# Kernel optimization log

Measured on AMD Instinct MI355X. Metric: run time of the kernel, lower is better.

The kernel has to match this reference:

```python
import jax, jax.numpy as jnp
import numpy as np

D_MODEL = 768
D_STATE = 16
D_CONV = 4
EXPAND = 2
D_INNER = EXPAND * D_MODEL  # 1536
BATCH = 2
SEQLEN = 4096


def setup_inputs() -> dict:
    key = jax.random.key(0)
    ks = jax.random.split(key, 8)
    s = 0.02
    return {
        "hidden_states": jax.random.normal(ks[0], (BATCH, SEQLEN, D_MODEL), jnp.float32),
        "W_in": jax.random.normal(ks[1], (D_MODEL, 2 * D_INNER), jnp.float32) * s,
        "conv_w": jax.random.normal(ks[2], (D_INNER, 1, D_CONV), jnp.float32) * s,
        "conv_b": jnp.zeros((D_INNER,), jnp.float32),
        "W_x": jax.random.normal(ks[3], (D_INNER, 2 * D_STATE + D_INNER), jnp.float32) * s,
        "W_dt": jax.random.normal(ks[4], (D_INNER, D_INNER), jnp.float32) * s,
        "b_dt": jnp.zeros((D_INNER,), jnp.float32),
        "A_log": jax.random.uniform(ks[5], (D_INNER, D_STATE), jnp.float32, minval=-1.0, maxval=0.0),
        "D": jnp.ones((D_INNER,), jnp.float32),
        "W_out": jax.random.normal(ks[6], (D_INNER, D_MODEL), jnp.float32) * s,
    }


def _silu(x):
    return x * jax.nn.sigmoid(x)


def reference(hidden_states, W_in, conv_w, conv_b, W_x, W_dt, b_dt, A_log, D, W_out):
    B, L, _ = hidden_states.shape
    # in_proj and split into x / gate z  (torch splits first half -> x, second -> z)
    xz = hidden_states @ W_in                      # (B, L, 2*ed)
    x, z = xz[..., :D_INNER], xz[..., D_INNER:]
    # causal depthwise conv1d (torch pads d_conv-1 both sides then truncates to L == left pad)
    xc = jnp.swapaxes(x, 1, 2)                     # (B, ed, L)
    xc = jax.lax.conv_general_dilated(
        xc, conv_w, window_strides=(1,), padding=[(D_CONV - 1, 0)],
        dimension_numbers=("NCH", "OIH", "NCH"), feature_group_count=D_INNER)
    x = jnp.swapaxes(xc, 1, 2) + conv_b            # (B, L, ed)
    x = _silu(x)
    # input-dependent SSM params
    xp = x @ W_x                                   # (B, L, 2*ds + ed)
    Bm = jax.nn.softmax(xp[..., :D_STATE], axis=-1)          # (B, L, ds)
    Cm = xp[..., D_STATE:2 * D_STATE]                          # (B, L, ds)
    delta = jax.nn.softplus(xp[..., 2 * D_STATE:] @ W_dt + b_dt)  # (B, L, ed)
    A = -jnp.exp(A_log.astype(jnp.float32))        # (ed, ds)

    def step(h, t):
        dt, Bt, Ct, ut = t                         # (B,ed),(B,ds),(B,ds),(B,ed)
        dA = jnp.exp(dt[:, :, None] * A)           # (B, ed, ds)
        h = dA * h + (dt[:, :, None] * Bt[:, None, :]) * ut[:, :, None]
        y = jnp.einsum('bs,bds->bd', Ct, h)        # (B, ed)
        return h, y

    h0 = jnp.zeros((B, D_INNER, D_STATE), x.dtype)
    ts = (jnp.swapaxes(delta, 0, 1), jnp.swapaxes(Bm, 0, 1),
          jnp.swapaxes(Cm, 0, 1), jnp.swapaxes(x, 0, 1))
    _, ys = jax.lax.scan(step, h0, ts)             # ys: (L, B, ed)
    y = jnp.swapaxes(ys, 0, 1)                     # (B, L, ed)
    # gating + out projection (torch fallback path does NOT add D * u)
    y = y * _silu(z)
    return y @ W_out
```

## Files before the change

### kernel.cpp

```cpp
#include <hip/hip_runtime.h>
#include <hip/hip_bf16.h>
#include <math.h>

#define D_MODEL 768
#define D_STATE 16
#define D_CONVW 4
#define D_INNER 1536
#define BATCH   2
#define SEQLEN  4096
#define NROWS   (BATCH*SEQLEN)
#define NCHUNK  128
#define LCHUNK  (SEQLEN/NCHUNK)

typedef __attribute__((ext_vector_type(8))) short short8;
typedef __attribute__((ext_vector_type(4))) float floatx4;

__device__ inline unsigned short f2b(float x) {
    unsigned u = __float_as_uint(x);
    return (unsigned short)((u + 0x7fffu + ((u >> 16) & 1u)) >> 16);
}
__device__ inline float b2f(unsigned short b) {
    return __uint_as_float(((unsigned)b) << 16);
}

#define GLDS(gp, lp) __builtin_amdgcn_global_load_lds( \
    (const __attribute__((address_space(1))) void*)(gp), \
    (__attribute__((address_space(3))) void*)(lp), 16, 0, 0)

template<int EPI, int OUTBF16>
__global__ __launch_bounds__(256, 4) void gemm_p2(
    const unsigned short* __restrict__ A, int lda,
    const unsigned short* __restrict__ Bt, int ldb,
    void* __restrict__ Cv, int ldc, float* __restrict__ C2,
    int N, int K, const float* __restrict__ bias, int nbx)
{
    __shared__ unsigned short As0[128*32], As1[128*32];
    __shared__ unsigned short Bs0[128*32], Bs1[128*32];

    const int nwg = gridDim.x;
    const int cpx = nwg >> 3;
    const int wg  = blockIdx.x;
    const int xcd = wg & 7, local = wg >> 3;
    int bmi, bni;
    if ((cpx % nbx == 0) && ((nbx & 1) == 0)) {
        const int R   = cpx / nbx;
        const int p   = local / (2 * R);
        const int idx = local % (2 * R);
        bmi = xcd * R + (idx >> 1);
        bni = p * 2 + (idx & 1);
    } else {
        const int swz = xcd * cpx + local;
        bmi = swz / nbx;
        bni = swz % nbx;
    }
    const int bm = bmi * 128;
    const int bn = bni * 128;

    const int tid  = threadIdx.x;
    const int lane = tid & 63;
    const int wave = tid >> 6;
    const int wm   = (wave >> 1) * 64;
    const int wn   = (wave & 1) * 64;
    const int l15  = lane & 15;
    const int lg   = lane >> 4;

    const int sr    = tid >> 2;
    const int sg    = ((tid & 3) ^ ((tid >> 3) & 3)) * 8;
    const int lbase = (tid & ~63) * 16;

    floatx4 acc[4][4] = {};

    auto stagePair = [&](unsigned short (&SA)[128*32],
                         unsigned short (&SB)[128*32], int kt) {
        #pragma unroll
        for (int p = 0; p < 2; ++p) {
            const unsigned short* ga = A + (size_t)(bm + p * 64 + sr) * lda + kt + sg;
            GLDS(ga, (char*)SA + p * 4096 + lbase);
        }
        #pragma unroll
        for (int p = 0; p < 2; ++p) {
            const unsigned short* gb = Bt + (size_t)(bn + p * 64 + sr) * ldb + kt + sg;
            GLDS(gb, (char*)SB + p * 4096 + lbase);
        }
    };

    auto compute = [&](const unsigned short (&CA)[128*32],
                       const unsigned short (&CB)[128*32]) {
        short8 af[4], bfv[4];
        #pragma unroll
        for (int i = 0; i < 4; ++i) {
            const int tr = wm + i * 16 + l15;
            const int ge = lg ^ ((tr >> 1) & 3);
            af[i] = *(const short8*)((const char*)CA + tr * 64 + ge * 16);
        }
        #pragma unroll
        for (int j = 0; j < 4; ++j) {
            const int tr = wn + j * 16 + l15;
            const int ge = lg ^ ((tr >> 1) & 3);
            bfv[j] = *(const short8*)((const char*)CB + tr * 64 + ge * 16);
        }
        #pragma unroll
        for (int i = 0; i < 4; ++i)
            #pragma unroll
            for (int j = 0; j < 4; ++j)
                acc[i][j] = __builtin_amdgcn_mfma_f32_16x16x32_bf16(
                    af[i], bfv[j], acc[i][j], 0, 0, 0);
    };

    const int NT = K >> 5;

    stagePair(As0, Bs0, 0);

    #define STEP(SA, SB, CA, CB, T)                                          \
    {                                                                        \
        const int t_ = (T);                                                  \
        if (t_ + 1 < NT) {                                                   \
            stagePair(SA, SB, (t_ + 1) * 32);                                \
            asm volatile("s_waitcnt vmcnt(4)" ::: "memory");                 \
        } else {                                                             \
            asm volatile("s_waitcnt vmcnt(0)" ::: "memory");                 \
        }                                                                    \
        __builtin_amdgcn_sched_barrier(0);                                   \
        __builtin_amdgcn_s_barrier();                                        \
        __builtin_amdgcn_sched_barrier(0);                                   \
        compute(CA, CB);                                                     \
        __builtin_amdgcn_sched_barrier(0);                                   \
        __builtin_amdgcn_s_barrier();                                        \
        __builtin_amdgcn_sched_barrier(0);                                   \
    }

    for (int t = 0; t < NT; t += 2) {
        STEP(As1, Bs1, As0, Bs0, t);
        STEP(As0, Bs0, As1, Bs1, t + 1);
    }
    #undef STEP

    #pragma unroll
    for (int i = 0; i < 4; ++i) {
        #pragma unroll
        for (int r = 0; r < 4; ++r) {
            const int gm = bm + wm + i * 16 + lg * 4 + r;
            #pragma unroll
            for (int j = 0; j < 4; ++j) {
                const int gn = bn + wn + j * 16 + l15;
                float v = acc[i][j][r];
                if (EPI == 3) {
                    if (gn < 32) {
                        C2[(size_t)gm * 32 + gn] = v;
                    } else if (gn < N) {
                        v += bias[gn - 32];
                        v = (v > 20.f) ? v : log1pf(__expf(v));
                        ((unsigned short*)Cv)[(size_t)gm * 1536 + gn - 32] = f2b(v);
                    }
                } else {
                    if (gn < N) {
                        if (OUTBF16)
                            ((unsigned short*)Cv)[(size_t)gm * ldc + gn] = f2b(v);
                        else
                            ((float*)Cv)[(size_t)gm * ldc + gn] = v;
                    }
                }
            }
        }
    }
}

__global__ __launch_bounds__(256) void transpose_bf16(
    const float* __restrict__ W, unsigned short* __restrict__ Wt, int K, int N)
{
    __shared__ float t[32][33];
    const int nt = blockIdx.x * 32, kt = blockIdx.y * 32;
    const int tx = threadIdx.x & 31, ty = threadIdx.x >> 5;
    #pragma unroll
    for (int r = 0; r < 4; ++r) {
        const int k = ty + r * 8;
        const int n = nt + tx;
        float v = 0.f;
        if (n < N) v = W[(size_t)(kt + k) * N + n];
        t[k][tx] = v;
    }
    __syncthreads();
    #pragma unroll
    for (int r = 0; r < 4; ++r) {
        const int nl = ty + r * 8;
        Wt[(size_t)(nt + nl) * K + kt + tx] = f2b(t[tx][nl]);
    }
}

__global__ __launch_bounds__(256) void f32_to_bf16(
    const float* __restrict__ in, unsigned short* __restrict__ o, int n4)
{
    const int i = blockIdx.x * 256 + threadIdx.x;
    if (i >= n4) return;
    float4 v = ((const float4*)in)[i];
    ushort4 r;
    r.x = f2b(v.x); r.y = f2b(v.y); r.z = f2b(v.z); r.w = f2b(v.w);
    ((ushort4*)o)[i] = r;
}

__global__ __launch_bounds__(256) void wx32_to_bf16(
    const float* __restrict__ Wx, unsigned short* __restrict__ o)
{
    const int i = blockIdx.x * 256 + threadIdx.x;
    if (i >= 1536 * 384) return;
    const int row = i / 384, q = i % 384;
    float4 v = *(const float4*)(Wx + (size_t)row * 1568 + 32 + q * 4);
    ushort4 r;
    r.x = f2b(v.x); r.y = f2b(v.y); r.z = f2b(v.z); r.w = f2b(v.w);
    *(ushort4*)(o + (size_t)row * 1536 + q * 4) = r;
}

__global__ __launch_bounds__(256) void conv_silu8(
    const unsigned short* __restrict__ xzb, const float* __restrict__ w,
    const float* __restrict__ cb, unsigned short* __restrict__ ub)
{
    const int i = blockIdx.x * 256 + threadIdx.x;
    if (i >= NROWS * 192) return;
    const int g   = i % 192;
    const int row = i / 192;
    const int l   = row % SEQLEN;
    const int d0  = g * 8;

    short8 xr[4];
    #pragma unroll
    for (int k = 0; k < 4; ++k) {
        const int ll = l - 3 + k;
        if (ll >= 0)
            xr[k] = *(const short8*)&xzb[(size_t)(row - 3 + k) * 3072 + d0];
        else
            xr[k] = short8{0,0,0,0,0,0,0,0};
    }
    unsigned short o[8];
    #pragma unroll
    for (int e = 0; e < 8; ++e) {
        float4 we = *(const float4*)&w[(d0 + e) * 4];
        float a = cb[d0 + e];
        a = fmaf(b2f((unsigned short)xr[0][e]), we.x, a);
        a = fmaf(b2f((unsigned short)xr[1][e]), we.y, a);
        a = fmaf(b2f((unsigned short)xr[2][e]), we.z, a);
        a = fmaf(b2f((unsigned short)xr[3][e]), we.w, a);
        o[e] = f2b(a / (1.f + __expf(-a)));
    }
    *(short8*)&ub[(size_t)row * 1536 + d0] = *(short8*)o;
}

__global__ __launch_bounds__(256) void softmax_bc_kernel(
    const float* __restrict__ xp32, float* __restrict__ Bsm, float* __restrict__ Csm)
{
    const int row = blockIdx.x * 256 + threadIdx.x;
    if (row >= NROWS) return;
    const float* p = xp32 + (size_t)row * 32;
    float v[16];
    #pragma unroll
    for (int q = 0; q < 4; ++q) {
        float4 t = *(const float4*)(p + q * 4);
        v[q*4+0]=t.x; v[q*4+1]=t.y; v[q*4+2]=t.z; v[q*4+3]=t.w;
    }
    float mx = v[0];
    #pragma unroll
    for (int s = 1; s < 16; ++s) mx = fmaxf(mx, v[s]);
    float sum = 0.f;
    #pragma unroll
    for (int s = 0; s < 16; ++s) { v[s] = __expf(v[s] - mx); sum += v[s]; }
    const float inv = 1.f / sum;
    float* bo = Bsm + (size_t)row * 16;
    float* co = Csm + (size_t)row * 16;
    #pragma unroll
    for (int s = 0; s < 16; ++s) bo[s] = v[s] * inv;
    #pragma unroll
    for (int q = 0; q < 4; ++q)
        *(float4*)(co + q * 4) = *(const float4*)(p + 16 + q * 4);
}

__global__ __launch_bounds__(256) void scan_chunk_state(
    const unsigned short* __restrict__ deltab, const unsigned short* __restrict__ ub,
    const float* __restrict__ Bsm, const float* __restrict__ A_log,
    float* __restrict__ chunkS, float* __restrict__ dtsum)
{
    const int gid = blockIdx.x * 256 + threadIdx.x;
    const int d = gid % D_INNER;
    const int c = (gid / D_INNER) % NCHUNK;
    const int b = gid / (D_INNER * NCHUNK);

    float A2[16];
    #pragma unroll
    for (int q = 0; q < 4; ++q) {
        float4 t = *(const float4*)(A_log + d * 16 + q * 4);
        A2[q*4+0] = -__expf(t.x) * 1.44269504089f;
        A2[q*4+1] = -__expf(t.y) * 1.44269504089f;
        A2[q*4+2] = -__expf(t.z) * 1.44269504089f;
        A2[q*4+3] = -__expf(t.w) * 1.44269504089f;
    }
    float h[16];
    #pragma unroll
    for (int s = 0; s < 16; ++s) h[s] = 0.f;
    float dts = 0.f;

    const int t0 = c * LCHUNK;
    for (int t = t0; t < t0 + LCHUNK; ++t) {
        const size_t rowoff = (size_t)b * SEQLEN + t;
        const float dt = b2f(deltab[rowoff * D_INNER + d]);
        const float uu = b2f(ub[rowoff * D_INNER + d]);
        const float du = dt * uu;
        dts += dt;
        const float4* Bp = (const float4*)(Bsm + rowoff * 16);
        float Bv[16];
        #pragma unroll
        for (int q = 0; q < 4; ++q) {
            float4 tb = Bp[q];
            Bv[q*4+0]=tb.x; Bv[q*4+1]=tb.y; Bv[q*4+2]=tb.z; Bv[q*4+3]=tb.w;
        }
        #pragma unroll
        for (int s = 0; s < 16; ++s) {
            const float dA = exp2f(dt * A2[s]);
            h[s] = fmaf(dA, h[s], du * Bv[s]);
        }
    }
    float* S = chunkS + (size_t)gid * 16;
    #pragma unroll
    for (int q = 0; q < 4; ++q)
        *(float4*)(S + q * 4) = make_float4(h[q*4+0], h[q*4+1], h[q*4+2], h[q*4+3]);
    dtsum[gid] = dts;
}

__global__ __launch_bounds__(256) void scan_chunk_scan(
    const float* __restrict__ A_log, const float* __restrict__ dtsum,
    float* __restrict__ chunkS)
{
    const int gid = blockIdx.x * 256 + threadIdx.x;
    if (gid >= BATCH * D_INNER * 16) return;
    const int s = gid % 16;
    const int d = (gid / 16) % D_INNER;
    const int b = gid / (16 * D_INNER);
    const float A2 = -__expf(A_log[d * 16 + s]) * 1.44269504089f;
    float hprev = 0.f;
    for (int c = 0; c < NCHUNK; ++c) {
        const size_t cidx = ((size_t)(b * NCHUNK + c) * D_INNER + d);
        const float P  = exp2f(A2 * dtsum[cidx]);
        const size_t idx = cidx * 16 + s;
        const float Sc = chunkS[idx];
        chunkS[idx] = hprev;
        hprev = fmaf(P, hprev, Sc);
    }
}

__global__ __launch_bounds__(256) void scan_output(
    const unsigned short* __restrict__ deltab, const unsigned short* __restrict__ ub,
    const float* __restrict__ Bsm, const float* __restrict__ Csm,
    const float* __restrict__ A_log, const float* __restrict__ chunkS,
    const unsigned short* __restrict__ xzb, unsigned short* __restrict__ yb)
{
    const int gid = blockIdx.x * 256 + threadIdx.x;
    const int d = gid % D_INNER;
    const int c = (gid / D_INNER) % NCHUNK;
    const int b = gid / (D_INNER * NCHUNK);

    float A2[16];
    #pragma unroll
    for (int q = 0; q < 4; ++q) {
        float4 t = *(const float4*)(A_log + d * 16 + q * 4);
        A2[q*4+0] = -__expf(t.x) * 1.44269504089f;
        A2[q*4+1] = -__expf(t.y) * 1.44269504089f;
        A2[q*4+2] = -__expf(t.z) * 1.44269504089f;
        A2[q*4+3] = -__expf(t.w) * 1.44269504089f;
    }
    float h[16];
    const float* S = chunkS + (size_t)gid * 16;
    #pragma unroll
    for (int q = 0; q < 4; ++q) {
        float4 t = *(const float4*)(S + q * 4);
        h[q*4+0]=t.x; h[q*4+1]=t.y; h[q*4+2]=t.z; h[q*4+3]=t.w;
    }

    const int t0 = c * LCHUNK;
    for (int t = t0; t < t0 + LCHUNK; ++t) {
        const size_t rowoff = (size_t)b * SEQLEN + t;
        const float dt = b2f(deltab[rowoff * D_INNER + d]);
        const float uu = b2f(ub[rowoff * D_INNER + d]);
        const float du = dt * uu;
        const float4* Bp = (const float4*)(Bsm + rowoff * 16);
        const float4* Cp = (const float4*)(Csm + rowoff * 16);
        float Bv[16], Cv[16];
        #pragma unroll
        for (int q = 0; q < 4; ++q) {
            float4 tb = Bp[q], tc = Cp[q];
            Bv[q*4+0]=tb.x; Bv[q*4+1]=tb.y; Bv[q*4+2]=tb.z; Bv[q*4+3]=tb.w;
            Cv[q*4+0]=tc.x; Cv[q*4+1]=tc.y; Cv[q*4+2]=tc.z; Cv[q*4+3]=tc.w;
        }
        float yv = 0.f;
        #pragma unroll
        for (int s = 0; s < 16; ++s) {
            const float dA = exp2f(dt * A2[s]);
            h[s] = fmaf(dA, h[s], du * Bv[s]);
            yv = fmaf(Cv[s], h[s], yv);
        }
        const float z = b2f(xzb[rowoff * (2 * D_INNER) + D_INNER + d]);
        const float sz = z / (1.f + __expf(-z));
        yb[rowoff * D_INNER + d] = f2b(yv * sz);
    }
}

extern "C" void kernel_launch(void* const* d_in, const int* in_sizes, int n_in,
                              void* d_out, int out_size, void* d_ws, size_t ws_size,
                              hipStream_t stream)
{
    const float* hs     = (const float*)d_in[0];
    const float* W_in   = (const float*)d_in[1];
    const float* conv_w = (const float*)d_in[2];
    const float* conv_b = (const float*)d_in[3];
    const float* W_x    = (const float*)d_in[4];
    const float* W_dt   = (const float*)d_in[5];
    const float* b_dt   = (const float*)d_in[6];
    const float* A_log  = (const float*)d_in[7];
    const float* W_out  = (const float*)d_in[9];
    float* out = (float*)d_out;

    char* w = (char*)d_ws;
    auto alloc = [&](size_t bytes) { char* p = w; w += (bytes + 255) & ~(size_t)255; return p; };
    float*          xp32   = (float*)alloc((size_t)NROWS * 32 * 4);
    unsigned short* deltab = (unsigned short*)alloc((size_t)NROWS * 1536 * 2);
    float*          Bsm    = (float*)alloc((size_t)NROWS * 16 * 4);
    float*          Csm    = (float*)alloc((size_t)NROWS * 16 * 4);
    float*          chunkS = (float*)alloc((size_t)BATCH * NCHUNK * D_INNER * 16 * 4);
    float*          dtsum  = (float*)alloc((size_t)BATCH * NCHUNK * D_INNER * 4);
    unsigned short* xzb    = (unsigned short*)alloc((size_t)NROWS * 3072 * 2);
    unsigned short* ub     = (unsigned short*)alloc((size_t)NROWS * 1536 * 2);
    unsigned short* yb     = (unsigned short*)alloc((size_t)NROWS * 1536 * 2);
    unsigned short* hsb    = (unsigned short*)alloc((size_t)NROWS * 768 * 2);
    unsigned short* Wt_in  = (unsigned short*)alloc((size_t)3072 * 768 * 2);
    unsigned short* Wt_x   = (unsigned short*)alloc((size_t)1792 * 1536 * 2);
    unsigned short* Wt_dt  = (unsigned short*)alloc((size_t)1536 * 1536 * 2);
    unsigned short* Wt_out = (unsigned short*)alloc((size_t)768 * 1536 * 2);
    unsigned short* wxb    = (unsigned short*)alloc((size_t)1536 * 1536 * 2);

    const dim3 blk(256);

    transpose_bf16<<<dim3(3072/32, 768/32),  blk, 0, stream>>>(W_in,  Wt_in,  768,  3072);
    transpose_bf16<<<dim3(1792/32, 1536/32), blk, 0, stream>>>(W_x,   Wt_x,   1536, 1568);
    transpose_bf16<<<dim3(1536/32, 1536/32), blk, 0, stream>>>(W_dt,  Wt_dt,  1536, 1536);
    transpose_bf16<<<dim3(768/32,  1536/32), blk, 0, stream>>>(W_out, Wt_out, 1536, 768);
    f32_to_bf16<<<(NROWS*768/4 + 255)/256, blk, 0, stream>>>(hs, hsb, NROWS*768/4);
    wx32_to_bf16<<<(1536*384 + 255)/256, blk, 0, stream>>>(W_x, wxb);

    gemm_p2<0,1><<<dim3(144), blk, 0, stream>>>(
        Wt_dt, 1536, wxb, 1536, Wt_x + (size_t)32 * 1536, 1536, nullptr,
        1536, 1536, nullptr, 12);

    gemm_p2<0,1><<<dim3(1536), blk, 0, stream>>>(
        hsb, 768, Wt_in, 768, xzb, 3072, nullptr, 3072, 768, nullptr, 24);

    conv_silu8<<<(NROWS*192)/256, blk, 0, stream>>>(xzb, conv_w, conv_b, ub);

    gemm_p2<3,0><<<dim3(896), blk, 0, stream>>>(
        ub, 1536, Wt_x, 1536, deltab, 1536, xp32, 1568, 1536, b_dt, 14);

    softmax_bc_kernel<<<NROWS/256, blk, 0, stream>>>(xp32, Bsm, Csm);

    scan_chunk_state<<<(BATCH*NCHUNK*D_INNER)/256, blk, 0, stream>>>(
        deltab, ub, Bsm, A_log, chunkS, dtsum);
    scan_chunk_scan<<<(BATCH*D_INNER*16 + 255)/256, blk, 0, stream>>>(
        A_log, dtsum, chunkS);
    scan_output<<<(BATCH*NCHUNK*D_INNER)/256, blk, 0, stream>>>(
        deltab, ub, Bsm, Csm, A_log, chunkS, xzb, yb);

    gemm_p2<0,0><<<dim3(384), blk, 0, stream>>>(
        yb, 1536, Wt_out, 1536, out, 768, nullptr, 768, 1536, nullptr, 6);
}
```

Measured before the change: 442.7 us.

## Add 8-wave 256x128 GEMM kernel for in_proj and x_proj GEMMs

Adds a gemm_w8 variant that runs 512 threads (8 waves) per block over a 256x128 output tile, using double-buffered LDS staging and one fewer outstanding load per stage. The original 4-wave 128x128 kernel is kept for the other GEMMs. The in_proj and x_proj/dt GEMMs switch to the new kernel, and the x_proj grid shrinks to 13 column tiles. The aim is to reuse each B tile across twice as many rows and so cut global and L2 traffic. In exchange each block uses more LDS, and the launch bound of 512 threads with 4 blocks may squeeze registers for the 64-float accumulator.

```diff
diff --git a/kernel.cpp b/kernel.cpp
--- a/kernel.cpp
+++ b/kernel.cpp
@@ -28,13 +28,13 @@
     (__attribute__((address_space(3))) void*)(lp), 16, 0, 0)
 
 template<int EPI, int OUTBF16>
-__global__ __launch_bounds__(256, 4) void gemm_p2(
+__global__ __launch_bounds__(512, 4) void gemm_w8(
     const unsigned short* __restrict__ A, int lda,
     const unsigned short* __restrict__ Bt, int ldb,
     void* __restrict__ Cv, int ldc, float* __restrict__ C2,
     int N, int K, const float* __restrict__ bias, int nbx)
 {
-    __shared__ unsigned short As0[128*32], As1[128*32];
+    __shared__ unsigned short As0[256*32], As1[256*32];
     __shared__ unsigned short Bs0[128*32], Bs1[128*32];
 
     const int nwg = gridDim.x;
@@ -53,7 +53,7 @@
         bmi = swz / nbx;
         bni = swz % nbx;
     }
-    const int bm = bmi * 128;
+    const int bm = bmi * 256;
     const int bn = bni * 128;
 
     const int tid  = threadIdx.x;
@@ -70,21 +70,18 @@
 
     floatx4 acc[4][4] = {};
 
-    auto stagePair = [&](unsigned short (&SA)[128*32],
+    auto stagePair = [&](unsigned short (&SA)[256*32],
                          unsigned short (&SB)[128*32], int kt) {
         #pragma unroll
-        for (int p = 0; p < 2; ++p) {
-            const unsigned short* ga = A + (size_t)(bm + p * 64 + sr) * lda + kt + sg;
-            GLDS(ga, (char*)SA + p * 4096 + lbase);
-        }
-        #pragma unroll
-        for (int p = 0; p < 2; ++p) {
-            const unsigned short* gb = Bt + (size_t)(bn + p * 64 + sr) * ldb + kt + sg;
-            GLDS(gb, (char*)SB + p * 4096 + lbase);
-        }
+        for (int q = 0; q < 2; ++q) {
+            const unsigned short* ga = A + (size_t)(bm + q * 128 + sr) * lda + kt + sg;
+            GLDS(ga, (char*)SA + q * 8192 + lbase);
+        }
+        const unsigned short* gb = Bt + (size_t)(bn + sr) * ldb + kt + sg;
+        GLDS(gb, (char*)SB + lbase);
     };
 
-    auto compute = [&](const unsigned short (&CA)[128*32],
+    auto compute = [&](const unsigned short (&CA)[256*32],
                        const unsigned short (&CB)[128*32]) {
         short8 af[4], bfv[4];
         #pragma unroll
@@ -116,7 +113,7 @@
         const int t_ = (T);                                                  \
         if (t_ + 1 < NT) {                                                   \
             stagePair(SA, SB, (t_ + 1) * 32);                                \
-            asm volatile("s_waitcnt vmcnt(4)" ::: "memory");                 \
+            asm volatile("s_waitcnt vmcnt(3)" ::: "memory");                 \
         } else {                                                             \
             asm volatile("s_waitcnt vmcnt(0)" ::: "memory");                 \
         }                                                                    \
@@ -165,6 +162,134 @@
     }
 }
 
+template<int EPI, int OUTBF16>
+__global__ __launch_bounds__(256, 4) void gemm_p2(
+    const unsigned short* __restrict__ A, int lda,
+    const unsigned short* __restrict__ Bt, int ldb,
+    void* __restrict__ Cv, int ldc, float* __restrict__ C2,
+    int N, int K, const float* __restrict__ bias, int nbx)
+{
+    __shared__ unsigned short As0[128*32], As1[128*32];
+    __shared__ unsigned short Bs0[128*32], Bs1[128*32];
+
+    const int nwg = gridDim.x;
+    const int cpx = nwg >> 3;
+    const int wg  = blockIdx.x;
+    const int xcd = wg & 7, local = wg >> 3;
+    int bmi, bni;
+    if ((cpx % nbx == 0) && ((nbx & 1) == 0)) {
+        const int R   = cpx / nbx;
+        const int p   = local / (2 * R);
+        const int idx = local % (2 * R);
+        bmi = xcd * R + (idx >> 1);
+        bni = p * 2 + (idx & 1);
+    } else {
+        const int swz = xcd * cpx + local;
+        bmi = swz / nbx;
+        bni = swz % nbx;
+    }
+    const int bm = bmi * 128;
+    const int bn = bni * 128;
+
+    const int tid  = threadIdx.x;
+    const int lane = tid & 63;
+    const int wave = tid >> 6;
+    const int wm   = (wave >> 1) * 64;
+    const int wn   = (wave & 1) * 64;
+    const int l15  = lane & 15;
+    const int lg   = lane >> 4;
+
+    const int sr    = tid >> 2;
+    const int sg    = ((tid & 3) ^ ((tid >> 3) & 3)) * 8;
+    const int lbase = (tid & ~63) * 16;
+
+    floatx4 acc[4][4] = {};
+
+    auto stagePair = [&](unsigned short (&SA)[128*32],
+                         unsigned short (&SB)[128*32], int kt) {
+        #pragma unroll
+        for (int p = 0; p < 2; ++p) {
+            const unsigned short* ga = A + (size_t)(bm + p * 64 + sr) * lda + kt + sg;
+            GLDS(ga, (char*)SA + p * 4096 + lbase);
+        }
+        #pragma unroll
+        for (int p = 0; p < 2; ++p) {
+            const unsigned short* gb = Bt + (size_t)(bn + p * 64 + sr) * ldb + kt + sg;
+            GLDS(gb, (char*)SB + p * 4096 + lbase);
+        }
+    };
+
+    auto compute = [&](const unsigned short (&CA)[128*32],
+                       const unsigned short (&CB)[128*32]) {
+        short8 af[4], bfv[4];
+        #pragma unroll
+        for (int i = 0; i < 4; ++i) {
+            const int tr = wm + i * 16 + l15;
+            const int ge = lg ^ ((tr >> 1) & 3);
+            af[i] = *(const short8*)((const char*)CA + tr * 64 + ge * 16);
+        }
+        #pragma unroll
+        for (int j = 0; j < 4; ++j) {
+            const int tr = wn + j * 16 + l15;
+            const int ge = lg ^ ((tr >> 1) & 3);
+            bfv[j] = *(const short8*)((const char*)CB + tr * 64 + ge * 16);
+        }
+        #pragma unroll
+        for (int i = 0; i < 4; ++i)
+            #pragma unroll
+            for (int j = 0; j < 4; ++j)
+                acc[i][j] = __builtin_amdgcn_mfma_f32_16x16x32_bf16(
+                    af[i], bfv[j], acc[i][j], 0, 0, 0);
+    };
+
+    const int NT = K >> 5;
+
+    stagePair(As0, Bs0, 0);
+
+    #define STEP(SA, SB, CA, CB, T)                                          \
+    {                                                                        \
+        const int t_ = (T);                                                  \
+        if (t_ + 1 < NT) {                                                   \
+            stagePair(SA, SB, (t_ + 1) * 32);                                \
+            asm volatile("s_waitcnt vmcnt(4)" ::: "memory");                 \
+        } else {                                                             \
+            asm volatile("s_waitcnt vmcnt(0)" ::: "memory");                 \
+        }                                                                    \
+        __builtin_amdgcn_sched_barrier(0);                                   \
+        __builtin_amdgcn_s_barrier();                                        \
+        __builtin_amdgcn_sched_barrier(0);                                   \
+        compute(CA, CB);                                                     \
+        __builtin_amdgcn_sched_barrier(0);                                   \
+        __builtin_amdgcn_s_barrier();                                        \
+        __builtin_amdgcn_sched_barrier(0);                                   \
+    }
+
+    for (int t = 0; t < NT; t += 2) {
+        STEP(As1, Bs1, As0, Bs0, t);
+        STEP(As0, Bs0, As1, Bs1, t + 1);
+    }
+    #undef STEP
+
+    #pragma unroll
+    for (int i = 0; i < 4; ++i) {
+        #pragma unroll
+        for (int r = 0; r < 4; ++r) {
+            const int gm = bm + wm + i * 16 + lg * 4 + r;
+            #pragma unroll
+            for (int j = 0; j < 4; ++j) {
+                const int gn = bn + wn + j * 16 + l15;
+                float v = acc[i][j][r];
+                if (gn < N) {
+                    if (OUTBF16)
+                        ((unsigned short*)Cv)[(size_t)gm * ldc + gn] = f2b(v);
+                    else
+                        ((float*)Cv)[(size_t)gm * ldc + gn] = v;
+                }
+            }
+        }
+    }
+}
+
 __global__ __launch_bounds__(256) void transpose_bf16(
     const float* __restrict__ W, unsigned short* __restrict__ Wt, int K, int N)
 {
@@ -446,13 +571,13 @@
         Wt_dt, 1536, wxb, 1536, Wt_x + (size_t)32 * 1536, 1536, nullptr,
         1536, 1536, nullptr, 12);
 
-    gemm_p2<0,1><<<dim3(1536), blk, 0, stream>>>(
+    gemm_w8<0,1><<<dim3(768), dim3(512), 0, stream>>>(
         hsb, 768, Wt_in, 768, xzb, 3072, nullptr, 3072, 768, nullptr, 24);
 
     conv_silu8<<<(NROWS*192)/256, blk, 0, stream>>>(xzb, conv_w, conv_b, ub);
 
-    gemm_p2<3,0><<<dim3(896), blk, 0, stream>>>(
-        ub, 1536, Wt_x, 1536, deltab, 1536, xp32, 1568, 1536, b_dt, 14);
+    gemm_w8<3,0><<<dim3(416), dim3(512), 0, stream>>>(
+        ub, 1536, Wt_x, 1536, deltab, 1536, xp32, 1568, 1536, b_dt, 13);
 
     softmax_bc_kernel<<<NROWS/256, blk, 0, stream>>>(xp32, Bsm, Csm);
 
```

Result: no change. 442.7 us (-0.0%).
